# Kernel optimization log

Hardware: AMD Instinct MI355X
Metric: run time of the kernel (lower is better)

Reference implementation:

```python
import jax, jax.numpy as jnp
import numpy as np
import math

D_MODEL = 1024
N_HEADS = 16
D_K = 64
CHUNK_LEN = 64


def setup_inputs() -> dict:
    key = jax.random.key(0)
    ks = jax.random.split(key, 12)
    hd = N_HEADS * D_K
    s = 0.02
    return {
        'h': jax.random.normal(ks[0], (4, 2048, D_MODEL), jnp.float32),
        'e': jax.random.normal(ks[1], (4, 32, 2, 128, D_MODEL), jnp.float32),
        'Wq': jax.random.normal(ks[2], (D_MODEL, hd), jnp.float32) * s,
        'bq': jnp.zeros((hd,), jnp.float32),
        'Wk': jax.random.normal(ks[3], (D_MODEL, hd), jnp.float32) * s,
        'bk': jnp.zeros((hd,), jnp.float32),
        'Wv': jax.random.normal(ks[4], (D_MODEL, hd), jnp.float32) * s,
        'bv': jnp.zeros((hd,), jnp.float32),
        'Wo': jax.random.normal(ks[5], (hd, D_MODEL), jnp.float32) * s,
        'bo': jnp.zeros((D_MODEL,), jnp.float32),
        'gamma': jnp.ones((D_MODEL,), jnp.float32),
        'beta': jnp.zeros((D_MODEL,), jnp.float32),
    }


def reference(h, e, Wq, bq, Wk, bk, Wv, bv, Wo, bo, gamma, beta):
    b, chunks, neighbors, nlen, d_model = e.shape
    seq_len = h.shape[1]
    scale = 1.0 / math.sqrt(D_K)
    h_res = h
    # shift so chunk i attends to neighbors retrieved for chunk i
    hh = h[:, CHUNK_LEN - 1:]
    # layer norm
    mu = jnp.mean(hh, axis=-1, keepdims=True)
    var = jnp.mean(jnp.square(hh - mu), axis=-1, keepdims=True)
    hh = (hh - mu) / jnp.sqrt(var + 1e-5) * gamma + beta
    # pad to chunks * CHUNK_LEN
    pad = chunks * CHUNK_LEN - hh.shape[1]
    hh = jnp.pad(hh, ((0, 0), (0, pad), (0, 0)))
    hh = hh.reshape(b, chunks, CHUNK_LEN, d_model)
    q = (hh @ Wq + bq).reshape(b, chunks, CHUNK_LEN, N_HEADS, D_K)
    k = (e @ Wk + bk).reshape(b, chunks, neighbors, nlen, N_HEADS, D_K)
    v = (e @ Wv + bv).reshape(b, chunks, neighbors, nlen, N_HEADS, D_K)
    attn = jnp.einsum('bcihd,bcnjhd->bchinj', q, k) * scale  # [b,c,h,i,n,j]
    a_shape = attn.shape
    attn = jax.nn.softmax(attn.reshape(*a_shape[:-2], -1), axis=-1).reshape(a_shape)
    out = jnp.einsum('bchinj,bcnjhd->bcihd', attn, v)
    out = out.reshape(b, chunks * CHUNK_LEN, N_HEADS * D_K)
    out = out @ Wo + bo
    out = jnp.pad(out, ((0, 0), (CHUNK_LEN - 1, 0), (0, 0)))
    return out[:, :seq_len] + h_res
```

## Files before the change

### kernel.cpp

```cpp
#include <hip/hip_runtime.h>
#include <cstdint>
#include <cstddef>


typedef float f32x4 __attribute__((ext_vector_type(4)));
typedef __bf16 bf16x8 __attribute__((ext_vector_type(8)));

static __device__ __forceinline__ ushort f2bf(float f) {
  union { float f; uint32_t u; } x; x.f = f;
  uint32_t r = x.u + 0x7fffu + ((x.u >> 16) & 1u);
  return (ushort)(r >> 16);
}

static __device__ __forceinline__ bf16x8 ld_frag(const ushort* p) {
  union { uint4 u; bf16x8 v; } x;
  x.u = *(const uint4*)p;
  return x.v;
}

static __device__ __forceinline__ void gl2lds16(const ushort* g, ushort* l) {
  __builtin_amdgcn_global_load_lds(
      (const __attribute__((address_space(1))) void*)g,
      (__attribute__((address_space(3))) void*)l,
      16, 0, 0);
}

__global__ __launch_bounds__(256) void transpose_cast4(const float* __restrict__ Wq,
                                                       const float* __restrict__ Wk,
                                                       const float* __restrict__ Wv,
                                                       const float* __restrict__ Wo,
                                                       ushort* __restrict__ WqT,
                                                       ushort* __restrict__ WkvT,
                                                       ushort* __restrict__ WoT) {
  const float* W; ushort* WT;
  switch (blockIdx.z) {
    case 0:  W = Wq; WT = WqT; break;
    case 1:  W = Wk; WT = WkvT; break;
    case 2:  W = Wv; WT = WkvT + (size_t)1024 * 1024; break;
    default: W = Wo; WT = WoT; break;
  }
  __shared__ float tile[64][65];
  const int t = threadIdx.x;
  const int n0 = blockIdx.x * 64, k0 = blockIdx.y * 64;
#pragma unroll
  for (int i = 0; i < 4; ++i) {
    int lid = i * 256 + t;
    int r = lid >> 4, c4 = (lid & 15) * 4;
    float4 v = *(const float4*)&W[(size_t)(k0 + r) * 1024 + n0 + c4];
    tile[r][c4 + 0] = v.x; tile[r][c4 + 1] = v.y;
    tile[r][c4 + 2] = v.z; tile[r][c4 + 3] = v.w;
  }
  __syncthreads();
#pragma unroll
  for (int i = 0; i < 4; ++i) {
    int lid = i * 256 + t;
    int n = lid >> 4, k4 = (lid & 15) * 4;
    ushort4 o;
    o.x = f2bf(tile[k4 + 0][n]); o.y = f2bf(tile[k4 + 1][n]);
    o.z = f2bf(tile[k4 + 2][n]); o.w = f2bf(tile[k4 + 3][n]);
    *(ushort4*)&WT[(size_t)(n0 + n) * 1024 + k0 + k4] = o;
  }
}

__global__ __launch_bounds__(256) void cast_bf16(const float* __restrict__ x,
                                                 ushort* __restrict__ y) {
  const size_t i = ((size_t)blockIdx.x * 256 + threadIdx.x) * 8;
  float4 a = *(const float4*)&x[i];
  float4 b = *(const float4*)&x[i + 4];
  ushort o[8];
  o[0] = f2bf(a.x); o[1] = f2bf(a.y); o[2] = f2bf(a.z); o[3] = f2bf(a.w);
  o[4] = f2bf(b.x); o[5] = f2bf(b.y); o[6] = f2bf(b.z); o[7] = f2bf(b.w);
  *(uint4*)&y[i] = *(const uint4*)o;
}

__global__ __launch_bounds__(256) void ln_kernel(const float* __restrict__ h,
                                                 const float* __restrict__ gamma,
                                                 const float* __restrict__ beta,
                                                 ushort* __restrict__ hh) {
  const int bx = blockIdx.x;
  const int b = bx >> 11, s = bx & 2047;
  const int t = threadIdx.x;
  ushort* orow = hh + (size_t)(b * 2048 + s) * 1024;
  if (s >= 1985) {
    ushort4 z; z.x = 0; z.y = 0; z.z = 0; z.w = 0;
    *(ushort4*)&orow[t * 4] = z;
    return;
  }
  const float* xrow = h + (size_t)(b * 2048 + 63 + s) * 1024;
  float4 x = *(const float4*)&xrow[t * 4];
  float s1 = x.x + x.y + x.z + x.w;
  float s2 = x.x * x.x + x.y * x.y + x.z * x.z + x.w * x.w;
#pragma unroll
  for (int off = 32; off > 0; off >>= 1) {
    s1 += __shfl_xor(s1, off);
    s2 += __shfl_xor(s2, off);
  }
  __shared__ float a1[4], a2[4];
  if ((t & 63) == 0) { a1[t >> 6] = s1; a2[t >> 6] = s2; }
  __syncthreads();
  s1 = a1[0] + a1[1] + a1[2] + a1[3];
  s2 = a2[0] + a2[1] + a2[2] + a2[3];
  const float mu = s1 * (1.0f / 1024.0f);
  const float var = s2 * (1.0f / 1024.0f) - mu * mu;
  const float rstd = rsqrtf(var + 1e-5f);
  float4 g = *(const float4*)&gamma[t * 4];
  float4 be = *(const float4*)&beta[t * 4];
  ushort4 o;
  o.x = f2bf((x.x - mu) * rstd * g.x + be.x);
  o.y = f2bf((x.y - mu) * rstd * g.y + be.y);
  o.z = f2bf((x.z - mu) * rstd * g.z + be.z);
  o.w = f2bf((x.w - mu) * rstd * g.w + be.w);
  *(ushort4*)&orow[t * 4] = o;
}

template <int MODE, int NT>
__global__ __launch_bounds__(256) void gemm_bf16(const ushort* __restrict__ A,
                                                 const ushort* __restrict__ Bt,
                                                 const float* __restrict__ bias,
                                                 const float* __restrict__ bias2,
                                                 ushort* __restrict__ Cbf,
                                                 ushort* __restrict__ Vtg,
                                                 float* __restrict__ Cf,
                                                 const float* __restrict__ resid,
                                                 int mtiles, float scale,
                                                 int mrow_off) {
  __shared__ __align__(16) ushort Alds[2][128 * 32];
  __shared__ __align__(16) ushort Blds[2][128 * 32];
  const int t = threadIdx.x;
  const int lane = t & 63, wave = t >> 6;
  const int quad = lane >> 4, l16 = lane & 15;

  const int L = blockIdx.x;
  const int xcd = L & 7, slot = L >> 3;
  const int nt = slot & (NT - 1);
  const int mt = xcd * (mtiles >> 3) + (slot / NT);
  const int m0 = mt * 128, n0 = nt * 128;

  const int srow = lane >> 2;
  const int scol = (lane & 3) * 8;
  const int c0 = wave * 2;
  const ushort* gA0 = A  + (size_t)(m0 + c0 * 16 + srow) * 1024 + scol;
  const ushort* gA1 = gA0 + 16 * 1024;
  const ushort* gB0 = Bt + (size_t)(n0 + c0 * 16 + srow) * 1024 + scol;
  const ushort* gB1 = gB0 + 16 * 1024;
  ushort* dA0 = &Alds[0][c0 * 512 + lane * 8];
  ushort* dA1 = dA0 + 512;
  ushort* dB0 = &Blds[0][c0 * 512 + lane * 8];
  ushort* dB1 = dB0 + 512;
  const ptrdiff_t SUB = 128 * 32;

  const int wrow = (wave >> 1) * 64, wcol = (wave & 1) * 64;
  const ushort* pA = &Alds[0][(wrow + l16) * 32 + quad * 8];
  const ushort* pB = &Blds[0][(wcol + l16) * 32 + quad * 8];

  f32x4 zero = {0.f, 0.f, 0.f, 0.f};
  f32x4 acc[4][4];
#pragma unroll
  for (int i = 0; i < 4; ++i)
#pragma unroll
    for (int j = 0; j < 4; ++j) acc[i][j] = zero;

  for (int kb = 0; kb < 16; ++kb) {
    const int ko = kb * 64;
    gl2lds16(gA0 + ko, dA0);         gl2lds16(gA1 + ko, dA1);
    gl2lds16(gA0 + ko + 32, dA0 + SUB); gl2lds16(gA1 + ko + 32, dA1 + SUB);
    gl2lds16(gB0 + ko, dB0);         gl2lds16(gB1 + ko, dB1);
    gl2lds16(gB0 + ko + 32, dB0 + SUB); gl2lds16(gB1 + ko + 32, dB1 + SUB);
    __syncthreads();
#pragma unroll
    for (int sub = 0; sub < 2; ++sub) {
      bf16x8 af[4], bfv[4];
#pragma unroll
      for (int i = 0; i < 4; ++i) af[i]  = ld_frag(pA + sub * SUB + i * 512);
#pragma unroll
      for (int j = 0; j < 4; ++j) bfv[j] = ld_frag(pB + sub * SUB + j * 512);
#pragma unroll
      for (int i = 0; i < 4; ++i)
#pragma unroll
        for (int j = 0; j < 4; ++j)
          acc[i][j] = __builtin_amdgcn_mfma_f32_16x16x32_bf16(af[i], bfv[j], acc[i][j], 0, 0, 0);
    }
    __syncthreads();
  }

#pragma unroll
  for (int mi = 0; mi < 4; ++mi)
#pragma unroll
    for (int mj = 0; mj < 4; ++mj) {
      const int cc = n0 + wcol + mj * 16 + l16;
      const int r0 = m0 + wrow + mi * 16 + quad * 4;
      if constexpr (MODE == 0) {
        const float bvb = bias[cc];
#pragma unroll
        for (int rr = 0; rr < 4; ++rr)
          Cbf[(size_t)(r0 + rr) * 1024 + cc] = f2bf((acc[mi][mj][rr] + bvb) * scale);
      } else if constexpr (MODE == 2) {
        if (nt < 8) {
          const float bvb = bias[cc];
#pragma unroll
          for (int rr = 0; rr < 4; ++rr)
            Cbf[(size_t)(r0 + rr) * 1024 + cc] = f2bf(acc[mi][mj][rr] + bvb);
        } else {
          const int cv = cc - 1024;
          const int hh_ = cv >> 6, dd = cv & 63;
          const float bvb = bias2[cv];
          const int gr0 = r0 + mrow_off;
          const int bcl = gr0 >> 8, j0 = gr0 & 255;
          ushort4 o;
          o.x = f2bf(acc[mi][mj][0] + bvb);
          o.y = f2bf(acc[mi][mj][1] + bvb);
          o.z = f2bf(acc[mi][mj][2] + bvb);
          o.w = f2bf(acc[mi][mj][3] + bvb);
          *(ushort4*)&Vtg[((size_t)(bcl * 16 + hh_)) * 16384 + dd * 256 + j0] = o;
        }
      } else {
        const float bvb = bias[cc];
#pragma unroll
        for (int rr = 0; rr < 4; ++rr) {
          const int r = r0 + rr;
          const int b = r >> 11, s = r & 2047;
          if (s < 1985) {
            const size_t o = (size_t)(b * 2048 + s + 63) * 1024 + cc;
            Cf[o] = acc[mi][mj][rr] + bvb + resid[o];
          }
        }
      }
    }
}

__global__ __launch_bounds__(256) void attn_kernel(const ushort* __restrict__ Qb,
                                                   const ushort* __restrict__ Kb,
                                                   const ushort* __restrict__ Vtg,
                                                   ushort* __restrict__ Ob) {
  __shared__ __align__(16) ushort smem[4608 + 18432 + 16896];
  __shared__ float redm[4][64];
  __shared__ float reds[4][64];
  ushort* Qs = smem;
  ushort* Ks = smem + 4608;
  ushort* Vt = smem + 23040;
  ushort* Ps = smem;

  const int t = threadIdx.x;
  const int bx = blockIdx.x;
  const int hd = bx & 15, c = (bx >> 4) & 31, b = bx >> 9;
  const int lane = t & 63, wave = t >> 6;
  const int quad = lane >> 4, l16 = lane & 15;

  const int qrow0 = b * 2048 + c * 64;
  const int kvrow0 = (b * 32 + c) * 256;
  const int colh = hd * 64;
  const ushort* vsrc = Vtg + ((size_t)((b * 32 + c) * 16 + hd)) * 16384;

#pragma unroll
  for (int it = 0; it < 2; ++it) {
    int lid = it * 256 + t;
    int r = lid >> 3, ch = (lid & 7) * 8;
    uint4 v = *(const uint4*)&Qb[(size_t)(qrow0 + r) * 1024 + colh + ch];
    *(uint4*)&Qs[r * 72 + ch] = v;
  }
#pragma unroll
  for (int it = 0; it < 8; ++it) {
    int lid = it * 256 + t;
    int r = lid >> 3, ch = (lid & 7) * 8;
    uint4 v = *(const uint4*)&Kb[(size_t)(kvrow0 + r) * 1024 + colh + ch];
    *(uint4*)&Ks[r * 72 + ch] = v;
  }
#pragma unroll
  for (int it = 0; it < 8; ++it) {
    int lid = it * 256 + t;
    int row = lid >> 5, c8 = (lid & 31) * 8;
    uint4 v = *(const uint4*)&vsrc[row * 256 + c8];
    *(uint4*)&Vt[row * 264 + c8] = v;
  }
  __syncthreads();

  const int jw = wave * 64;
  f32x4 zero = {0.f, 0.f, 0.f, 0.f};
  f32x4 acc[4][4];
#pragma unroll
  for (int i = 0; i < 4; ++i)
#pragma unroll
    for (int j = 0; j < 4; ++j) acc[i][j] = zero;

#pragma unroll
  for (int kb = 0; kb < 2; ++kb) {
    bf16x8 af[4], bfv[4];
#pragma unroll
    for (int mi = 0; mi < 4; ++mi)
      af[mi] = ld_frag(&Qs[(mi * 16 + l16) * 72 + kb * 32 + quad * 8]);
#pragma unroll
    for (int mj = 0; mj < 4; ++mj)
      bfv[mj] = ld_frag(&Ks[(jw + mj * 16 + l16) * 72 + kb * 32 + quad * 8]);
#pragma unroll
    for (int mi = 0; mi < 4; ++mi)
#pragma unroll
      for (int mj = 0; mj < 4; ++mj)
        acc[mi][mj] = __builtin_amdgcn_mfma_f32_16x16x32_bf16(af[mi], bfv[mj], acc[mi][mj], 0, 0, 0);
  }

  float rmax[4][4];
#pragma unroll
  for (int mi = 0; mi < 4; ++mi)
#pragma unroll
    for (int rr = 0; rr < 4; ++rr) {
      float m = fmaxf(fmaxf(acc[mi][0][rr], acc[mi][1][rr]),
                      fmaxf(acc[mi][2][rr], acc[mi][3][rr]));
      m = fmaxf(m, __shfl_xor(m, 1));
      m = fmaxf(m, __shfl_xor(m, 2));
      m = fmaxf(m, __shfl_xor(m, 4));
      m = fmaxf(m, __shfl_xor(m, 8));
      rmax[mi][rr] = m;
    }
  if (l16 == 0) {
#pragma unroll
    for (int mi = 0; mi < 4; ++mi)
#pragma unroll
      for (int rr = 0; rr < 4; ++rr)
        redm[wave][mi * 16 + quad * 4 + rr] = rmax[mi][rr];
  }
  __syncthreads();
  float gmax[4][4];
#pragma unroll
  for (int mi = 0; mi < 4; ++mi)
#pragma unroll
    for (int rr = 0; rr < 4; ++rr) {
      const int row = mi * 16 + quad * 4 + rr;
      gmax[mi][rr] = fmaxf(fmaxf(redm[0][row], redm[1][row]),
                           fmaxf(redm[2][row], redm[3][row]));
    }
  float rsum[4][4];
#pragma unroll
  for (int mi = 0; mi < 4; ++mi)
#pragma unroll
    for (int rr = 0; rr < 4; ++rr) {
      float s = 0.f;
#pragma unroll
      for (int mj = 0; mj < 4; ++mj) {
        float p = exp2f((acc[mi][mj][rr] - gmax[mi][rr]) * 1.4426950408889634f);
        acc[mi][mj][rr] = p;
        s += p;
      }
      s += __shfl_xor(s, 1);
      s += __shfl_xor(s, 2);
      s += __shfl_xor(s, 4);
      s += __shfl_xor(s, 8);
      rsum[mi][rr] = s;
    }
  if (l16 == 0) {
#pragma unroll
    for (int mi = 0; mi < 4; ++mi)
#pragma unroll
      for (int rr = 0; rr < 4; ++rr)
        reds[wave][mi * 16 + quad * 4 + rr] = rsum[mi][rr];
  }
  __syncthreads();
#pragma unroll
  for (int mi = 0; mi < 4; ++mi)
#pragma unroll
    for (int rr = 0; rr < 4; ++rr) {
      const int row = mi * 16 + quad * 4 + rr;
      const float inv = 1.0f / (reds[0][row] + reds[1][row] + reds[2][row] + reds[3][row]);
#pragma unroll
      for (int mj = 0; mj < 4; ++mj)
        Ps[row * 264 + jw + mj * 16 + l16] = f2bf(acc[mi][mj][rr] * inv);
    }
  __syncthreads();

  const int d0 = wave * 16;
  f32x4 acc2[4];
#pragma unroll
  for (int mi = 0; mi < 4; ++mi) acc2[mi] = zero;
#pragma unroll
  for (int kb = 0; kb < 8; ++kb) {
    bf16x8 bfv = ld_frag(&Vt[(d0 + l16) * 264 + kb * 32 + quad * 8]);
#pragma unroll
    for (int mi = 0; mi < 4; ++mi) {
      bf16x8 af = ld_frag(&Ps[(mi * 16 + l16) * 264 + kb * 32 + quad * 8]);
      acc2[mi] = __builtin_amdgcn_mfma_f32_16x16x32_bf16(af, bfv, acc2[mi], 0, 0, 0);
    }
  }
#pragma unroll
  for (int mi = 0; mi < 4; ++mi)
#pragma unroll
    for (int rr = 0; rr < 4; ++rr) {
      const int i = mi * 16 + quad * 4 + rr;
      Ob[(size_t)(qrow0 + i) * 1024 + colh + d0 + l16] = f2bf(acc2[mi][rr]);
    }
}

__global__ __launch_bounds__(256) void head_copy(const float* __restrict__ h,
                                                 float* __restrict__ out) {
  const int idx4 = blockIdx.x * 256 + threadIdx.x;
  const int b = idx4 / 16128;
  const int rem = idx4 - b * 16128;
  const size_t o = (size_t)b * 2048 * 1024 + (size_t)rem * 4;
  *(float4*)&out[o] = *(const float4*)&h[o];
}

extern "C" void kernel_launch(void* const* d_in, const int* in_sizes, int n_in,
                              void* d_out, int out_size, void* d_ws, size_t ws_size,
                              hipStream_t stream) {
  const float* h     = (const float*)d_in[0];
  const float* e     = (const float*)d_in[1];
  const float* Wq    = (const float*)d_in[2];
  const float* bq    = (const float*)d_in[3];
  const float* Wk    = (const float*)d_in[4];
  const float* bk    = (const float*)d_in[5];
  const float* Wv    = (const float*)d_in[6];
  const float* bv    = (const float*)d_in[7];
  const float* Wo    = (const float*)d_in[8];
  const float* bo    = (const float*)d_in[9];
  const float* gamma = (const float*)d_in[10];
  const float* beta  = (const float*)d_in[11];
  float* out = (float*)d_out;

  char* ws = (char*)d_ws;
  ushort* stg  = (ushort*)(ws + ((size_t)0 << 20));
  ushort* WqT  = (ushort*)(ws + ((size_t)32 << 20));
  ushort* WkvT = (ushort*)(ws + ((size_t)34 << 20));
  ushort* WoT  = (ushort*)(ws + ((size_t)38 << 20));
  ushort* Qb   = (ushort*)(ws + ((size_t)40 << 20));
  ushort* Kb   = (ushort*)(ws + ((size_t)56 << 20));
  ushort* VtG  = (ushort*)(ws + ((size_t)120 << 20));

  transpose_cast4<<<dim3(16, 16, 4), 256, 0, stream>>>(Wq, Wk, Wv, Wo, WqT, WkvT, WoT);

  ln_kernel<<<8192, 256, 0, stream>>>(h, gamma, beta, stg);

  gemm_bf16<0, 8><<<512, 256, 0, stream>>>(stg, WqT, bq, nullptr, Qb, nullptr,
                                           nullptr, nullptr, 64, 0.125f, 0);

  for (int half = 0; half < 2; ++half) {
    const size_t roff = (size_t)half * 16384 * 1024;
    cast_bf16<<<8192, 256, 0, stream>>>(e + roff, stg);
    gemm_bf16<2, 16><<<2048, 256, 0, stream>>>(stg, WkvT, bk, bv, Kb + roff,
                                               VtG, nullptr, nullptr,
                                               128, 1.0f, half * 16384);
  }

  attn_kernel<<<2048, 256, 0, stream>>>(Qb, Kb, VtG, stg);

  gemm_bf16<1, 8><<<512, 256, 0, stream>>>(stg, WoT, bo, nullptr, nullptr, nullptr,
                                           out, h, 64, 1.0f, 0);
  head_copy<<<252, 256, 0, stream>>>(h, out);
}
```

Measured before the change: 558.4 us.

## Replace K/V projection GEMM with 256x256-tile 8-wave pipelined kernel

Adds a dedicated K/V projection GEMM using 256x256 output tiles, 512 threads, XCD-aware block mapping, swizzled direct global-to-LDS loads, and a double-buffered schedule that interleaves staging with MFMA phases under explicit barriers and setprio. The goal is more data reuse per tile and better overlap of memory traffic with matrix math than the generic 128-wide gemm_bf16 path offered. The price is high register pressure (an 8x4 accumulator array per wave, 128 KB of LDS per block) and fragile hand-tuned wait counts.

```diff
diff --git a/kernel.cpp b/kernel.cpp
--- a/kernel.cpp
+++ b/kernel.cpp
@@ -194,25 +194,6 @@
 #pragma unroll
         for (int rr = 0; rr < 4; ++rr)
           Cbf[(size_t)(r0 + rr) * 1024 + cc] = f2bf((acc[mi][mj][rr] + bvb) * scale);
-      } else if constexpr (MODE == 2) {
-        if (nt < 8) {
-          const float bvb = bias[cc];
-#pragma unroll
-          for (int rr = 0; rr < 4; ++rr)
-            Cbf[(size_t)(r0 + rr) * 1024 + cc] = f2bf(acc[mi][mj][rr] + bvb);
-        } else {
-          const int cv = cc - 1024;
-          const int hh_ = cv >> 6, dd = cv & 63;
-          const float bvb = bias2[cv];
-          const int gr0 = r0 + mrow_off;
-          const int bcl = gr0 >> 8, j0 = gr0 & 255;
-          ushort4 o;
-          o.x = f2bf(acc[mi][mj][0] + bvb);
-          o.y = f2bf(acc[mi][mj][1] + bvb);
-          o.z = f2bf(acc[mi][mj][2] + bvb);
-          o.w = f2bf(acc[mi][mj][3] + bvb);
-          *(ushort4*)&Vtg[((size_t)(bcl * 16 + hh_)) * 16384 + dd * 256 + j0] = o;
-        }
       } else {
         const float bvb = bias[cc];
 #pragma unroll
@@ -226,6 +207,189 @@
         }
       }
     }
+}
+
+__global__ __launch_bounds__(512, 2) void gemm_kv256(const ushort* __restrict__ A,
+                                                     const ushort* __restrict__ Bt,
+                                                     const float* __restrict__ bk_,
+                                                     const float* __restrict__ bv_,
+                                                     ushort* __restrict__ Kout,
+                                                     ushort* __restrict__ Vtg,
+                                                     int mrow_off) {
+  __shared__ __align__(16) ushort Alds[4 * 8192];
+  __shared__ __align__(16) ushort Blds[4 * 8192];
+
+  const int t = threadIdx.x;
+  const int lane = t & 63, wave = t >> 6;
+  const int wm = wave >> 2, wn = wave & 3;
+  const int l16 = lane & 15, quad = lane >> 4;
+
+  const int L = blockIdx.x;
+  const int xcd = L & 7, slot = L >> 3;
+  const int nt = slot & 7, mt = xcd * 8 + (slot >> 3);
+  const int m0 = mt * 256, n0 = nt * 256;
+
+  const int w2 = wave * 2;
+  const int srow = lane >> 3;
+  const int lanex = (lane & 7) ^ srow;
+  const ushort* gA2 = A  + (size_t)(m0 + w2 * 8 + srow) * 1024 + lanex * 8;
+  const ushort* gB2 = Bt + (size_t)(n0 + w2 * 8 + srow) * 1024 + lanex * 8;
+  ushort* dA2 = Alds + w2 * 512 + lane * 8;
+  ushort* dB2 = Blds + w2 * 512 + lane * 8;
+
+  auto stage_a = [&](int ti, int hh) {
+    const ushort* g = gA2 + (size_t)hh * 131072 + (size_t)ti * 64;
+    ushort* d = dA2 + ((ti & 1) * 2 + hh) * 8192;
+    gl2lds16(g, d);
+    gl2lds16(g + 8192, d + 512);
+  };
+  auto stage_b = [&](int ti, int hh) {
+    const ushort* g = gB2 + (size_t)hh * 131072 + (size_t)ti * 64;
+    ushort* d = dB2 + ((ti & 1) * 2 + hh) * 8192;
+    gl2lds16(g, d);
+    gl2lds16(g + 8192, d + 512);
+  };
+
+  const int b2 = (l16 >> 2) & 1;
+  const int qx = (quad ^ (l16 & 3)) << 3;
+  const int kof0 = b2 << 5;
+  const int kof1 = 32 - kof0;
+
+  f32x4 zero = {0.f, 0.f, 0.f, 0.f};
+  f32x4 acc[8][4];
+#pragma unroll
+  for (int i = 0; i < 8; ++i)
+#pragma unroll
+    for (int j = 0; j < 4; ++j) acc[i][j] = zero;
+
+  stage_b(0, 0); stage_a(0, 0); stage_b(0, 1); stage_a(0, 1);
+  stage_b(1, 0); stage_a(1, 0); stage_b(1, 1);
+  asm volatile("s_waitcnt vmcnt(6)" ::: "memory");
+  __builtin_amdgcn_s_barrier();
+
+  bf16x8 a[4][2], b01[2][2], b23[2][2];
+
+#pragma unroll 2
+  for (int tt = 0; tt < 16; ++tt) {
+    const int cur = tt & 1;
+    const ushort* pa = Alds + (cur * 2 + wm) * 8192 + l16 * 64 + qx;
+    const ushort* pb = Blds + (cur * 2 + (wn >> 1)) * 8192 +
+                       ((wn & 1) * 64 + l16) * 64 + qx;
+
+#pragma unroll
+    for (int mi = 0; mi < 4; ++mi) {
+      a[mi][0] = ld_frag(pa + mi * 1024 + kof0);
+      a[mi][1] = ld_frag(pa + mi * 1024 + kof1);
+    }
+#pragma unroll
+    for (int ni = 0; ni < 2; ++ni) {
+      b01[ni][0] = ld_frag(pb + ni * 1024 + kof0);
+      b01[ni][1] = ld_frag(pb + ni * 1024 + kof1);
+    }
+    if (tt < 15) stage_a(tt + 1, 1);
+    __builtin_amdgcn_s_barrier();
+    asm volatile("s_waitcnt lgkmcnt(0)" ::: "memory");
+    __builtin_amdgcn_sched_barrier(0);
+    __builtin_amdgcn_s_setprio(1);
+#pragma unroll
+    for (int mi = 0; mi < 4; ++mi)
+#pragma unroll
+      for (int ni = 0; ni < 2; ++ni) {
+        acc[mi][ni] = __builtin_amdgcn_mfma_f32_16x16x32_bf16(a[mi][0], b01[ni][0], acc[mi][ni], 0, 0, 0);
+        acc[mi][ni] = __builtin_amdgcn_mfma_f32_16x16x32_bf16(a[mi][1], b01[ni][1], acc[mi][ni], 0, 0, 0);
+      }
+    __builtin_amdgcn_s_setprio(0);
+    __builtin_amdgcn_s_barrier();
+
+#pragma unroll
+    for (int ni = 0; ni < 2; ++ni) {
+      b23[ni][0] = ld_frag(pb + (ni + 2) * 1024 + kof0);
+      b23[ni][1] = ld_frag(pb + (ni + 2) * 1024 + kof1);
+    }
+    __builtin_amdgcn_s_barrier();
+    asm volatile("s_waitcnt lgkmcnt(0)" ::: "memory");
+    __builtin_amdgcn_sched_barrier(0);
+    __builtin_amdgcn_s_setprio(1);
+#pragma unroll
+    for (int mi = 0; mi < 4; ++mi)
+#pragma unroll
+      for (int ni = 0; ni < 2; ++ni) {
+        acc[mi][ni + 2] = __builtin_amdgcn_mfma_f32_16x16x32_bf16(a[mi][0], b23[ni][0], acc[mi][ni + 2], 0, 0, 0);
+        acc[mi][ni + 2] = __builtin_amdgcn_mfma_f32_16x16x32_bf16(a[mi][1], b23[ni][1], acc[mi][ni + 2], 0, 0, 0);
+      }
+    __builtin_amdgcn_s_setprio(0);
+    __builtin_amdgcn_s_barrier();
+
+#pragma unroll
+    for (int mi = 0; mi < 4; ++mi) {
+      a[mi][0] = ld_frag(pa + (mi + 4) * 1024 + kof0);
+      a[mi][1] = ld_frag(pa + (mi + 4) * 1024 + kof1);
+    }
+    if (tt < 14) stage_b(tt + 2, 0);
+    __builtin_amdgcn_s_barrier();
+    asm volatile("s_waitcnt lgkmcnt(0)" ::: "memory");
+    __builtin_amdgcn_sched_barrier(0);
+    __builtin_amdgcn_s_setprio(1);
+#pragma unroll
+    for (int mi = 0; mi < 4; ++mi)
+#pragma unroll
+      for (int ni = 0; ni < 2; ++ni) {
+        acc[mi + 4][ni + 2] = __builtin_amdgcn_mfma_f32_16x16x32_bf16(a[mi][0], b23[ni][0], acc[mi + 4][ni + 2], 0, 0, 0);
+        acc[mi + 4][ni + 2] = __builtin_amdgcn_mfma_f32_16x16x32_bf16(a[mi][1], b23[ni][1], acc[mi + 4][ni + 2], 0, 0, 0);
+      }
+    __builtin_amdgcn_s_setprio(0);
+    __builtin_amdgcn_s_barrier();
+
+    if (tt < 14) { stage_a(tt + 2, 0); stage_b(tt + 2, 1); }
+    __builtin_amdgcn_s_barrier();
+    __builtin_amdgcn_s_setprio(1);
+#pragma unroll
+    for (int mi = 0; mi < 4; ++mi)
+#pragma unroll
+      for (int ni = 0; ni < 2; ++ni) {
+        acc[mi + 4][ni] = __builtin_amdgcn_mfma_f32_16x16x32_bf16(a[mi][0], b01[ni][0], acc[mi + 4][ni], 0, 0, 0);
+        acc[mi + 4][ni] = __builtin_amdgcn_mfma_f32_16x16x32_bf16(a[mi][1], b01[ni][1], acc[mi + 4][ni], 0, 0, 0);
+      }
+    __builtin_amdgcn_s_setprio(0);
+    if (tt < 15) {
+      if (tt == 14) asm volatile("s_waitcnt vmcnt(0)" ::: "memory");
+      else          asm volatile("s_waitcnt vmcnt(6)" ::: "memory");
+      __builtin_amdgcn_s_barrier();
+    }
+  }
+
+  const int rbase = m0 + wm * 128 + quad * 4;
+  const int cbase = n0 + wn * 64 + l16;
+  if (n0 < 1024) {
+#pragma unroll
+    for (int mi = 0; mi < 8; ++mi)
+#pragma unroll
+      for (int ni = 0; ni < 4; ++ni) {
+        const int cc = cbase + ni * 16;
+        const float bb = bk_[cc];
+        const int r0 = rbase + mi * 16;
+#pragma unroll
+        for (int rr = 0; rr < 4; ++rr)
+          Kout[(size_t)(r0 + rr) * 1024 + cc] = f2bf(acc[mi][ni][rr] + bb);
+      }
+  } else {
+#pragma unroll
+    for (int mi = 0; mi < 8; ++mi)
+#pragma unroll
+      for (int ni = 0; ni < 4; ++ni) {
+        const int cv = cbase - 1024 + ni * 16;
+        const int hh_ = cv >> 6, dd = cv & 63;
+        const float bb = bv_[cv];
+        const int gr0 = rbase + mi * 16 + mrow_off;
+        const int bcl = gr0 >> 8, j0 = gr0 & 255;
+        ushort4 o;
+        o.x = f2bf(acc[mi][ni][0] + bb);
+        o.y = f2bf(acc[mi][ni][1] + bb);
+        o.z = f2bf(acc[mi][ni][2] + bb);
+        o.w = f2bf(acc[mi][ni][3] + bb);
+        *(ushort4*)&Vtg[(size_t)(bcl * 16 + hh_) * 16384 + dd * 256 + j0] = o;
+      }
+  }
 }
 
 __global__ __launch_bounds__(256) void attn_kernel(const ushort* __restrict__ Qb,
@@ -433,9 +597,8 @@
   for (int half = 0; half < 2; ++half) {
     const size_t roff = (size_t)half * 16384 * 1024;
     cast_bf16<<<8192, 256, 0, stream>>>(e + roff, stg);
-    gemm_bf16<2, 16><<<2048, 256, 0, stream>>>(stg, WkvT, bk, bv, Kb + roff,
-                                               VtG, nullptr, nullptr,
-                                               128, 1.0f, half * 16384);
+    gemm_kv256<<<512, 512, 0, stream>>>(stg, WkvT, bk, bv, Kb + roff,
+                                        VtG, half * 16384);
   }
 
   attn_kernel<<<2048, 256, 0, stream>>>(Qb, Kb, VtG, stg);
```

Result: faster. 524.0 us (-6.2%).
